# Performance work log

Measured on AMD Instinct MI355X. Metric: run time of the kernel, lower is better.

The kernel has to match this reference:

```python
import jax, jax.numpy as jnp
import numpy as np

B, F, T, H, K = 512, 64, 64, 512, 4  # batch, in_feat, timesteps, hidden, num cells (air0,bed0,air1,bed1)


def setup_inputs() -> dict:
    key = jax.random.key(0)
    ks = jax.random.split(key, 10)
    s = 1.0 / np.sqrt(H)
    u = lambda k, shape: jax.random.uniform(k, shape, jnp.float32, -s, s)
    return {
        "data": jax.random.normal(ks[0], (B, F, T), jnp.float32),
        "init": jax.random.normal(ks[1], (B, H), jnp.float32),
        # stacked params for the 4 branches in order [air0, bed0, air1, bed1]
        "fc_in_W": u(ks[2], (K, H, F)),
        "fc_in_b": u(ks[3], (K, H)),
        "Wih": u(ks[4], (K, 3 * H, H)),   # torch GRUCell weight_ih, gate order r,z,n
        "Whh": u(ks[5], (K, 3 * H, H)),
        "bih": u(ks[6], (K, 3 * H)),
        "bhh": u(ks[7], (K, 3 * H)),
        "fc_out_W": u(ks[8], (2, H)),     # [air, bed] output heads (Linear(512,1))
        "fc_out_b": u(ks[9], (2,)),
    }


def reference(data, init, fc_in_W, fc_in_b, Wih, Whh, bih, bhh, fc_out_W, fc_out_b):
    # Input projections (Linear + ReLU; Dropout is identity in eval): [T, K, B, H]
    proj = jax.nn.relu(jnp.einsum('bft,kof->tkbo', data, fc_in_W) + fc_in_b[None, :, None, :])
    # branches 2,3 (air1, bed1) consume the sequence reversed (data[:, :, 63-i])
    x_seq = jnp.concatenate([proj[:, :2], proj[::-1, 2:]], axis=1)  # [T, K, B, H]

    h0 = jnp.broadcast_to(init[None], (K,) + init.shape)  # all 4 cells start from init

    def step(h, x):  # h, x: [K, B, H]
        gi = jnp.einsum('kbi,koi->kbo', x, Wih) + bih[:, None, :]
        gh = jnp.einsum('kbi,koi->kbo', h, Whh) + bhh[:, None, :]
        ir, iz, inn = jnp.split(gi, 3, axis=-1)
        hr, hz, hn = jnp.split(gh, 3, axis=-1)
        r = jax.nn.sigmoid(ir + hr)
        z = jax.nn.sigmoid(iz + hz)
        n = jnp.tanh(inn + r * hn)
        h_new = (1.0 - z) * n + z * h
        return h_new, h_new

    _, hs = jax.lax.scan(step, h0, x_seq)  # [T, K, B, H]

    # output i (1..64) combines fwd hidden[i] with bwd hidden[65-i] -> reverse bwd stack
    air = hs[:, 0] + hs[::-1, 2]  # [T, B, H]
    bed = hs[:, 1] + hs[::-1, 3]
    air_out = (jnp.einsum('tbh,h->tb', air, fc_out_W[0]) + fc_out_b[0]).T  # [B, T]
    bed_out = (jnp.einsum('tbh,h->tb', bed, fc_out_W[1]) + fc_out_b[1]).T
    return air_out, bed_out
```

## Files before the change

### kernel.cpp

```cpp
#include <hip/hip_runtime.h>
#include <hip/hip_bf16.h>

typedef __hip_bfloat16 bf16;
typedef __attribute__((ext_vector_type(8))) short short8;
typedef __attribute__((ext_vector_type(4))) float f32x4;

#define Hdim 512
#define Bdim 512
#define Tdim 64
#define Fdim 64
#define NC   4

__device__ __forceinline__ float sigmoidf_(float x){ return 1.f/(1.f + __expf(-x)); }
__device__ __forceinline__ float tanhf_(float x){
  float t = __expf(-2.f*fabsf(x));
  float r = (1.f - t)/(1.f + t);
  return copysignf(r, x);
}
__device__ __forceinline__ float bf2f_(short u){
  return __uint_as_float(((unsigned)(unsigned short)u) << 16);
}
__device__ __forceinline__ short f2bf_(float f){
  bf16 b = (bf16)f;
  return *(short*)&b;
}

__global__ __launch_bounds__(256) void pack_kernel(const float* __restrict__ src,
                                                   bf16* __restrict__ dst, int n){
  int idx = (blockIdx.x*256 + threadIdx.x)*4;
  if (idx < n){
    float4 v = *(const float4*)(src + idx);
    dst[idx+0] = (bf16)v.x;
    dst[idx+1] = (bf16)v.y;
    dst[idx+2] = (bf16)v.z;
    dst[idx+3] = (bf16)v.w;
  }
}

__global__ __launch_bounds__(256) void transpose_kernel(const float* __restrict__ data,
                                                        bf16* __restrict__ dataT){
  __shared__ bf16 tile[64*65];
  int b = blockIdx.x;
  int tid = threadIdx.x;
  for (int i = 0; i < 16; ++i){
    int idx = tid + i*256;
    int f = idx >> 6, t = idx & 63;
    tile[f*65 + t] = (bf16)data[(b*64 + f)*64 + t];
  }
  __syncthreads();
  for (int i = 0; i < 16; ++i){
    int idx = tid + i*256;
    int t = idx >> 6, f = idx & 63;
    dataT[(t*Bdim + b)*64 + f] = tile[f*65 + t];
  }
}

__global__ __launch_bounds__(256) void init_kernel(const float* __restrict__ init_h,
                            bf16* __restrict__ h_b1, unsigned* __restrict__ flags){
  int idx = blockIdx.x*256 + threadIdx.x;
  int k = idx >> 18;
  int rem = idx & 262143;
  int bg = rem >> 9;
  int o  = rem & 511;
  int dst = ((k*2 + (bg >> 8))*16 + (o >> 5))*8192 + (bg & 255)*32 + (o & 31);
  h_b1[dst] = (bf16)init_h[rem];
  if (idx < 512) flags[idx] = 0u;
}

__global__ __launch_bounds__(256) void proj_kernel(const bf16* __restrict__ dataT,
    const bf16* __restrict__ fc_in_W, const float* __restrict__ fc_in_b,
    bf16* __restrict__ x_seq){
  __shared__ short ldsA[64*72];
  __shared__ short ldsW[128*72];
  int blk = blockIdx.x;
  int s  = blk >> 7;
  int k  = (blk >> 5) & 3;
  int bt = (blk >> 2) & 7;
  int on = blk & 3;
  int tid = threadIdx.x;
  int lane = tid & 63, wid = tid >> 6;
  int quad = lane >> 4, l16 = lane & 15;
  int src_t = (k < 2) ? s : (Tdim - 1 - s);

  const short* Ag = (const short*)(dataT + (src_t*Bdim + bt*64)*Fdim);
  #pragma unroll
  for (int i = 0; i < 2; ++i){
    int c = tid + i*256; int r = c >> 3, off = c & 7;
    *(int4*)(&ldsA[r*72 + off*8]) = *(const int4*)(&Ag[r*64 + off*8]);
  }
  const short* Wg = (const short*)(fc_in_W + (k*Hdim + on*128)*Fdim);
  #pragma unroll
  for (int i = 0; i < 4; ++i){
    int c = tid + i*256; int r = c >> 3, off = c & 7;
    *(int4*)(&ldsW[r*72 + off*8]) = *(const int4*)(&Wg[r*64 + off*8]);
  }
  __syncthreads();

  f32x4 acc[2][4];
  #pragma unroll
  for (int nt=0; nt<2; ++nt)
    #pragma unroll
    for (int rb=0; rb<4; ++rb) acc[nt][rb] = (f32x4){0.f,0.f,0.f,0.f};

  #pragma unroll
  for (int kk = 0; kk < 2; ++kk){
    int io = kk*32 + quad*8;
    short8 a[4];
    #pragma unroll
    for (int rb=0; rb<4; ++rb) a[rb] = *(const short8*)(&ldsA[(rb*16+l16)*72 + io]);
    #pragma unroll
    for (int nt=0; nt<2; ++nt){
      short8 bw = *(const short8*)(&ldsW[(wid*32 + nt*16 + l16)*72 + io]);
      #pragma unroll
      for (int rb=0; rb<4; ++rb)
        acc[nt][rb] = __builtin_amdgcn_mfma_f32_16x16x32_bf16(a[rb], bw, acc[nt][rb], 0,0,0);
    }
  }

  #pragma unroll
  for (int nt=0; nt<2; ++nt){
    int o = on*128 + wid*32 + nt*16 + l16;
    float bias = fc_in_b[k*Hdim + o];
    #pragma unroll
    for (int rb=0; rb<4; ++rb){
      #pragma unroll
      for (int reg=0; reg<4; ++reg){
        int b = bt*64 + rb*16 + quad*4 + reg;
        float v = acc[nt][rb][reg] + bias;
        v = v > 0.f ? v : 0.f;
        x_seq[((size_t)(s*NC + k)*Bdim + b)*Hdim + o] = (bf16)v;
      }
    }
  }
}

__global__ __launch_bounds__(512) void rnn_kernel(
    const bf16* __restrict__ x_seq, const float* __restrict__ init_h,
    bf16* __restrict__ h_b0, bf16* __restrict__ h_b1,
    const float* __restrict__ Wih, const float* __restrict__ Whh,
    const float* __restrict__ bih, const float* __restrict__ bhh,
    const float* __restrict__ fc_out_W,
    bf16* __restrict__ gi, float* __restrict__ part,
    unsigned* __restrict__ flags, unsigned* __restrict__ xslot)
{
  __shared__ short wlds[3*2*16*512];
  __shared__ int sslot;

  int tid = threadIdx.x;
  int lane = tid & 63, wid = tid >> 6;
  int quad = lane >> 4, l16 = lane & 15;

  unsigned xcc;
  asm volatile("s_getreg_b32 %0, hwreg(HW_REG_XCC_ID)" : "=s"(xcc));
  xcc &= 7u;
  if (tid == 0)
    sslot = (int)__hip_atomic_fetch_add(&xslot[xcc*32], 1u,
                __ATOMIC_RELAXED, __HIP_MEMORY_SCOPE_WORKGROUP);
  __syncthreads();
  int grp = (int)xcc;
  int k   = grp >> 1;
  int bt  = grp & 1;
  int slot = sslot & 31;
  int producer = (slot < 16);
  int j    = slot & 15;
  int obase = j*32;
  int rot  = j;
  unsigned* gflags = flags + grp*32;

  const float* Wsrc = producer ? Wih : Whh;
  for (int i = tid; i < 3*2*16*64; i += 512){
    int plane = i >> 11;
    int rem   = i & 2047;
    int nt    = rem >> 10;
    int rem2  = rem & 1023;
    int kc    = rem2 >> 6;
    int ln    = rem2 & 63;
    int ll16  = ln & 15, lq = ln >> 4;
    const float* srcp = Wsrc +
        ((size_t)(k*3 + plane)*Hdim + obase + nt*16 + ll16)*Hdim + kc*32 + lq*8;
    float4 f0 = *(const float4*)srcp;
    float4 f1 = *(const float4*)(srcp + 4);
    short8 pk;
    pk[0]=f2bf_(f0.x); pk[1]=f2bf_(f0.y); pk[2]=f2bf_(f0.z); pk[3]=f2bf_(f0.w);
    pk[4]=f2bf_(f1.x); pk[5]=f2bf_(f1.y); pk[6]=f2bf_(f1.z); pk[7]=f2bf_(f1.w);
    *(int4*)(&wlds[i*8]) = *(int4*)&pk;
  }

  #define GEMM32X(ABASE) do {                                                   \
    const short* ap0_ = (ABASE) + (wid*32 + l16)*Hdim + quad*8;                 \
    const short* ap1_ = ap0_ + 16*Hdim;                                         \
    short8 ab_[4][2];                                                           \
    _Pragma("unroll")                                                           \
    for (int d=0; d<4; ++d){                                                    \
      int c_ = (d + rot) & 15;                                                  \
      ab_[d][0] = *(const short8*)(ap0_ + c_*32);                               \
      ab_[d][1] = *(const short8*)(ap1_ + c_*32);                               \
    }                                                                           \
    short8 bb_[2][6];                                                           \
    _Pragma("unroll")                                                           \
    for (int p=0; p<6; ++p)                                                     \
      bb_[0][p] = *(const short8*)(&wlds[((p*16 + rot)<<9) + (lane<<3)]);       \
    _Pragma("unroll")                                                           \
    for (int kc=0; kc<16; ++kc){                                                \
      short8 a0_ = ab_[kc&3][0], a1_ = ab_[kc&3][1];                            \
      if (kc < 12){                                                             \
        int c_ = (kc + 4 + rot) & 15;                                           \
        ab_[kc&3][0] = *(const short8*)(ap0_ + c_*32);                          \
        ab_[kc&3][1] = *(const short8*)(ap1_ + c_*32);                          \
      }                                                                         \
      if (kc < 15){                                                             \
        int c_ = (kc + 1 + rot) & 15;                                           \
        _Pragma("unroll")                                                       \
        for (int p=0; p<6; ++p)                                                 \
          bb_[(kc+1)&1][p] = *(const short8*)(&wlds[((p*16 + c_)<<9) + (lane<<3)]); \
      }                                                                         \
      _Pragma("unroll")                                                         \
      for (int g=0; g<3; ++g){                                                  \
        _Pragma("unroll")                                                       \
        for (int nt=0; nt<2; ++nt){                                             \
          short8 bw_ = bb_[kc&1][g*2+nt];                                       \
          acc[g][nt][0] = __builtin_amdgcn_mfma_f32_16x16x32_bf16(a0_, bw_, acc[g][nt][0], 0,0,0); \
          acc[g][nt][1] = __builtin_amdgcn_mfma_f32_16x16x32_bf16(a1_, bw_, acc[g][nt][1], 0,0,0); \
        }                                                                       \
      }                                                                         \
    }                                                                           \
  } while(0)

  #define GEMM32H(HCB) do {                                                     \
    const short* hp0_ = (HCB) + (wid*32 + l16)*32 + quad*8;                     \
    const short* hp1_ = hp0_ + 16*32;                                           \
    short8 ab_[4][2];                                                           \
    _Pragma("unroll")                                                           \
    for (int d=0; d<4; ++d){                                                    \
      int c_ = (d + rot) & 15;                                                  \
      ab_[d][0] = *(const short8*)(hp0_ + c_*8192);                             \
      ab_[d][1] = *(const short8*)(hp1_ + c_*8192);                             \
    }                                                                           \
    short8 bb_[2][6];                                                           \
    _Pragma("unroll")                                                           \
    for (int p=0; p<6; ++p)                                                     \
      bb_[0][p] = *(const short8*)(&wlds[((p*16 + rot)<<9) + (lane<<3)]);       \
    _Pragma("unroll")                                                           \
    for (int kc=0; kc<16; ++kc){                                                \
      short8 a0_ = ab_[kc&3][0], a1_ = ab_[kc&3][1];                            \
      if (kc < 12){                                                             \
        int c_ = (kc + 4 + rot) & 15;                                           \
        ab_[kc&3][0] = *(const short8*)(hp0_ + c_*8192);                        \
        ab_[kc&3][1] = *(const short8*)(hp1_ + c_*8192);                        \
      }                                                                         \
      if (kc < 15){                                                             \
        int c_ = (kc + 1 + rot) & 15;                                           \
        _Pragma("unroll")                                                       \
        for (int p=0; p<6; ++p)                                                 \
          bb_[(kc+1)&1][p] = *(const short8*)(&wlds[((p*16 + c_)<<9) + (lane<<3)]); \
      }                                                                         \
      _Pragma("unroll")                                                         \
      for (int g=0; g<3; ++g){                                                  \
        _Pragma("unroll")                                                       \
        for (int nt=0; nt<2; ++nt){                                             \
          short8 bw_ = bb_[kc&1][g*2+nt];                                       \
          acc[g][nt][0] = __builtin_amdgcn_mfma_f32_16x16x32_bf16(a0_, bw_, acc[g][nt][0], 0,0,0); \
          acc[g][nt][1] = __builtin_amdgcn_mfma_f32_16x16x32_bf16(a1_, bw_, acc[g][nt][1], 0,0,0); \
        }                                                                       \
      }                                                                         \
    }                                                                           \
  } while(0)

  if (producer){
    __syncthreads();
    for (int s = 0; s < 64; ++s){
      f32x4 acc[3][2][2];
      #pragma unroll
      for (int g=0; g<3; ++g)
        #pragma unroll
        for (int nt=0; nt<2; ++nt){
          acc[g][nt][0] = (f32x4){0.f,0.f,0.f,0.f};
          acc[g][nt][1] = (f32x4){0.f,0.f,0.f,0.f};
        }
      if (s >= 3){
        if (wid == 0){
          int g_ = 0;
          while (__hip_atomic_load(&gflags[16 + j], __ATOMIC_RELAXED,
                                   __HIP_MEMORY_SCOPE_AGENT) < (unsigned)(s - 2)){
            __builtin_amdgcn_s_sleep(1);
            if (++g_ > 4000000) break;
          }
        }
        __syncthreads();
      }
      const short* x_base = (const short*)(x_seq + ((size_t)(s*NC + k)*Bdim + bt*256)*Hdim);
      GEMM32X(x_base);
      bf16* gb = gi + ((size_t)(((s % 3)*8 + grp)*16 + j))*24576;
      #pragma unroll
      for (int g=0; g<3; ++g){
        #pragma unroll
        for (int nt=0; nt<2; ++nt){
          short8 pk;
          #pragma unroll
          for (int rb=0; rb<2; ++rb)
            #pragma unroll
            for (int reg=0; reg<4; ++reg)
              pk[rb*4+reg] = f2bf_(acc[g][nt][rb][reg]);
          *(int4*)(gb + ((g*2+nt)*512 + wid*64 + lane)*8) = *(int4*)&pk;
        }
      }
      __syncthreads();
      if (tid == 0)
        __hip_atomic_fetch_add(&gflags[j], 1u,
                               __ATOMIC_RELAXED, __HIP_MEMORY_SCOPE_AGENT);
    }
  } else {
    int o0 = obase + l16, o1 = o0 + 16;
    float br0  = bih[k*3*Hdim + o0] + bhh[k*3*Hdim + o0];
    float br1  = bih[k*3*Hdim + o1] + bhh[k*3*Hdim + o1];
    float bz0  = bih[k*3*Hdim + Hdim + o0] + bhh[k*3*Hdim + Hdim + o0];
    float bz1  = bih[k*3*Hdim + Hdim + o1] + bhh[k*3*Hdim + Hdim + o1];
    float bnx0 = bih[k*3*Hdim + 2*Hdim + o0];
    float bnx1 = bih[k*3*Hdim + 2*Hdim + o1];
    float bnh0 = bhh[k*3*Hdim + 2*Hdim + o0];
    float bnh1 = bhh[k*3*Hdim + 2*Hdim + o1];
    float wout0 = fc_out_W[(k & 1)*Hdim + o0];
    float wout1 = fc_out_W[(k & 1)*Hdim + o1];

    float hk[2][2][4];
    #pragma unroll
    for (int nt=0; nt<2; ++nt)
      #pragma unroll
      for (int rb=0; rb<2; ++rb)
        #pragma unroll
        for (int reg=0; reg<4; ++reg)
          hk[nt][rb][reg] =
            init_h[(bt*256 + wid*32 + rb*16 + quad*4 + reg)*Hdim + obase + nt*16 + l16];

    __syncthreads();

    const int hgrp = (k*2 + bt)*16;

    for (int s = 0; s < 64; ++s){
      const bf16* h_in  = (s & 1) ? h_b0 : h_b1;
      bf16*       h_out = (s & 1) ? h_b1 : h_b0;

      f32x4 acc[3][2][2];
      #pragma unroll
      for (int g=0; g<3; ++g)
        #pragma unroll
        for (int nt=0; nt<2; ++nt){
          acc[g][nt][0] = (f32x4){0.f,0.f,0.f,0.f};
          acc[g][nt][1] = (f32x4){0.f,0.f,0.f,0.f};
        }

      {
        if (wid == 0){
          int g_ = 0;
          for (;;){
            unsigned v_ = 0xFFFFFFFFu, thr_ = 0u;
            if (lane < 16){
              v_ = __hip_atomic_load(&gflags[16 + lane], __ATOMIC_RELAXED,
                                     __HIP_MEMORY_SCOPE_AGENT);
              thr_ = (unsigned)s;
            } else if (lane == 16){
              v_ = __hip_atomic_load(&gflags[j], __ATOMIC_RELAXED,
                                     __HIP_MEMORY_SCOPE_AGENT);
              thr_ = (unsigned)(s + 1);
            }
            if (__ballot(v_ >= thr_) == ~0ull) break;
            __builtin_amdgcn_s_sleep(1);
            if (++g_ > 4000000) break;
          }
        }
        __syncthreads();
      }

      const bf16* gb = gi + ((size_t)(((s % 3)*8 + grp)*16 + j))*24576;
      short8 gv[6];
      #pragma unroll
      for (int p=0; p<6; ++p){
        int4 t = *(const int4*)(gb + (p*512 + wid*64 + lane)*8);
        gv[p] = *(short8*)&t;
      }

      const short* h_cb = (const short*)h_in + (size_t)hgrp*8192;
      GEMM32H(h_cb);

      float hnv[2][2][4];
      bf16* hob = h_out + (size_t)(hgrp + j)*8192;
      #pragma unroll
      for (int rb = 0; rb < 2; ++rb){
        #pragma unroll
        for (int reg = 0; reg < 4; ++reg){
          int bl = wid*32 + rb*16 + quad*4 + reg;
          #pragma unroll
          for (int nt = 0; nt < 2; ++nt){
            float gir = bf2f_(gv[0*2+nt][rb*4+reg]);
            float giz = bf2f_(gv[1*2+nt][rb*4+reg]);
            float gin = bf2f_(gv[2*2+nt][rb*4+reg]);
            float br  = nt ? br1 : br0,  bz = nt ? bz1 : bz0;
            float bnx = nt ? bnx1 : bnx0, bnh = nt ? bnh1 : bnh0;
            float r = sigmoidf_(gir + acc[0][nt][rb][reg] + br);
            float z = sigmoidf_(giz + acc[1][nt][rb][reg] + bz);
            float n = tanhf_(gin + bnx + r*(acc[2][nt][rb][reg] + bnh));
            float hn = (1.f - z)*n + z*hk[nt][rb][reg];
            hk[nt][rb][reg] = hn;
            hnv[nt][rb][reg] = hn;
            hob[bl*32 + nt*16 + l16] = (bf16)hn;
          }
        }
      }

      __syncthreads();
      if (tid == 0)
        __hip_atomic_fetch_add(&gflags[16 + j], 1u,
                               __ATOMIC_RELAXED, __HIP_MEMORY_SCOPE_AGENT);

      int tmap = (k < 2) ? s : (Tdim - 1 - s);
      #pragma unroll
      for (int rb = 0; rb < 2; ++rb){
        #pragma unroll
        for (int reg = 0; reg < 4; ++reg){
          int bl = wid*32 + rb*16 + quad*4 + reg;
          float v = hnv[0][rb][reg]*wout0 + hnv[1][rb][reg]*wout1;
          v += __shfl_xor(v, 1, 64);
          v += __shfl_xor(v, 2, 64);
          v += __shfl_xor(v, 4, 64);
          v += __shfl_xor(v, 8, 64);
          if (l16 == 0)
            __builtin_nontemporal_store(v,
              &part[((size_t)(k*Tdim + tmap)*16 + j)*Bdim + bt*256 + bl]);
        }
      }
    }
  }
  #undef GEMM32X
  #undef GEMM32H
}

__global__ __launch_bounds__(256) void finalize_kernel(const float* __restrict__ part,
                                const float* __restrict__ fc_out_b, float* __restrict__ out){
  int idx = blockIdx.x*256 + threadIdx.x;
  int head = idx >> 15;
  int b = (idx >> 6) & 511;
  int t = idx & 63;
  float v = fc_out_b[head];
  #pragma unroll
  for (int kk = 0; kk < 2; ++kk){
    const float* p = part + (size_t)((head + kk*2)*Tdim + t)*16*Bdim + b;
    #pragma unroll
    for (int jj = 0; jj < 16; ++jj)
      v += p[jj*Bdim];
  }
  out[idx] = v;
}

extern "C" void kernel_launch(void* const* d_in, const int* in_sizes, int n_in,
                              void* d_out, int out_size, void* d_ws, size_t ws_size,
                              hipStream_t stream){
  (void)in_sizes; (void)n_in; (void)out_size; (void)ws_size;
  const float* data     = (const float*)d_in[0];
  const float* init_h   = (const float*)d_in[1];
  const float* fc_in_W  = (const float*)d_in[2];
  const float* fc_in_b  = (const float*)d_in[3];
  const float* Wih      = (const float*)d_in[4];
  const float* Whh      = (const float*)d_in[5];
  const float* bih      = (const float*)d_in[6];
  const float* bhh      = (const float*)d_in[7];
  const float* fc_out_W = (const float*)d_in[8];
  const float* fc_out_b = (const float*)d_in[9];
  float* out = (float*)d_out;

  char* ws = (char*)d_ws;
  bf16*  x_seq   = (bf16*)ws;
  bf16*  h_b0    = (bf16*)(ws + 134217728);
  bf16*  h_b1    = (bf16*)(ws + 136314880);
  bf16*  gi      = (bf16*)(ws + 138412032);
  bf16*  dataT   = (bf16*)(ws + 138412032);
  float* part    = (float*)(ws + 157286400);
  bf16*  fcW_bf  = (bf16*)(ws + 165675008);
  unsigned* flags= (unsigned*)(ws + 165937152);
  unsigned* xslot= (unsigned*)(ws + 165938176);

  const int nFW = NC*Hdim*Fdim;
  hipLaunchKernelGGL(pack_kernel, dim3(nFW/1024), dim3(256), 0, stream, fc_in_W, fcW_bf, nFW);
  hipLaunchKernelGGL(init_kernel, dim3(4096), dim3(256), 0, stream, init_h, h_b1, flags);
  hipLaunchKernelGGL(transpose_kernel, dim3(512), dim3(256), 0, stream, data, dataT);
  hipLaunchKernelGGL(proj_kernel, dim3(8192), dim3(256), 0, stream, dataT, fcW_bf, fc_in_b, x_seq);
  hipLaunchKernelGGL(rnn_kernel, dim3(256), dim3(512), 0, stream,
      x_seq, init_h, h_b0, h_b1, Wih, Whh, bih, bhh, fc_out_W, gi, part, flags, xslot);
  hipLaunchKernelGGL(finalize_kernel, dim3(256), dim3(256), 0, stream, part, fc_out_b, out);
}
```

Before: 743.4 us.

## Retile GRU GEMM warps to 64 rows by 16 cols, shrink gi ring

Each warp now computes a 64-row by 16-column tile instead of 32 by 32. That makes each warp load 3 LDS weight fragments per k-chunk instead of 6, while the A-side register loads double. The gi buffer ring drops from three slots to two, which tightens the producer/consumer flag thresholds. The consumer now waits for its own gi slot before the hidden-state barrier and prefetches gi during that wait. The partial-output layout doubles to 32 slices, so the finalize reduction and the workspace offsets change to match.

```diff
diff --git a/kernel.cpp b/kernel.cpp
--- a/kernel.cpp
+++ b/kernel.cpp
@@ -3,6 +3,7 @@
 
 typedef __hip_bfloat16 bf16;
 typedef __attribute__((ext_vector_type(8))) short short8;
+typedef __attribute__((ext_vector_type(4))) short short4_t;
 typedef __attribute__((ext_vector_type(4))) float f32x4;
 
 #define Hdim 512
@@ -148,6 +149,8 @@
 
   int tid = threadIdx.x;
   int lane = tid & 63, wid = tid >> 6;
+  int wgrp = wid >> 2;
+  int wsub = wid & 3;
   int quad = lane >> 4, l16 = lane & 15;
 
   unsigned xcc;
@@ -186,102 +189,64 @@
     *(int4*)(&wlds[i*8]) = *(int4*)&pk;
   }
 
-  #define GEMM32X(ABASE) do {                                                   \
-    const short* ap0_ = (ABASE) + (wid*32 + l16)*Hdim + quad*8;                 \
-    const short* ap1_ = ap0_ + 16*Hdim;                                         \
-    short8 ab_[4][2];                                                           \
+  #define GEMMNT(APFX, ROWSTRIDE, CSTRIDE) do {                                 \
+    const short* ap_[4];                                                        \
+    _Pragma("unroll")                                                           \
+    for (int rb=0; rb<4; ++rb)                                                  \
+      ap_[rb] = (APFX) + (wsub*64 + rb*16 + l16)*(ROWSTRIDE) + quad*8;          \
+    short8 ab_[4][4];                                                           \
     _Pragma("unroll")                                                           \
     for (int d=0; d<4; ++d){                                                    \
       int c_ = (d + rot) & 15;                                                  \
-      ab_[d][0] = *(const short8*)(ap0_ + c_*32);                               \
-      ab_[d][1] = *(const short8*)(ap1_ + c_*32);                               \
+      _Pragma("unroll")                                                         \
+      for (int rb=0; rb<4; ++rb)                                                \
+        ab_[d][rb] = *(const short8*)(ap_[rb] + (size_t)c_*(CSTRIDE));          \
     }                                                                           \
-    short8 bb_[2][6];                                                           \
+    short8 bb_[2][3];                                                           \
     _Pragma("unroll")                                                           \
-    for (int p=0; p<6; ++p)                                                     \
-      bb_[0][p] = *(const short8*)(&wlds[((p*16 + rot)<<9) + (lane<<3)]);       \
+    for (int g=0; g<3; ++g)                                                     \
+      bb_[0][g] = *(const short8*)(&wlds[((((g*2+wgrp)*16) + rot)<<9) + (lane<<3)]); \
     _Pragma("unroll")                                                           \
     for (int kc=0; kc<16; ++kc){                                                \
-      short8 a0_ = ab_[kc&3][0], a1_ = ab_[kc&3][1];                            \
+      short8 a_[4];                                                             \
+      _Pragma("unroll")                                                         \
+      for (int rb=0; rb<4; ++rb) a_[rb] = ab_[kc&3][rb];                        \
       if (kc < 12){                                                             \
         int c_ = (kc + 4 + rot) & 15;                                           \
-        ab_[kc&3][0] = *(const short8*)(ap0_ + c_*32);                          \
-        ab_[kc&3][1] = *(const short8*)(ap1_ + c_*32);                          \
+        _Pragma("unroll")                                                       \
+        for (int rb=0; rb<4; ++rb)                                              \
+          ab_[kc&3][rb] = *(const short8*)(ap_[rb] + (size_t)c_*(CSTRIDE));     \
       }                                                                         \
       if (kc < 15){                                                             \
         int c_ = (kc + 1 + rot) & 15;                                           \
         _Pragma("unroll")                                                       \
-        for (int p=0; p<6; ++p)                                                 \
-          bb_[(kc+1)&1][p] = *(const short8*)(&wlds[((p*16 + c_)<<9) + (lane<<3)]); \
+        for (int g=0; g<3; ++g)                                                 \
+          bb_[(kc+1)&1][g] =                                                    \
+            *(const short8*)(&wlds[((((g*2+wgrp)*16) + c_)<<9) + (lane<<3)]);   \
       }                                                                         \
       _Pragma("unroll")                                                         \
       for (int g=0; g<3; ++g){                                                  \
+        short8 bw_ = bb_[kc&1][g];                                              \
         _Pragma("unroll")                                                       \
-        for (int nt=0; nt<2; ++nt){                                             \
-          short8 bw_ = bb_[kc&1][g*2+nt];                                       \
-          acc[g][nt][0] = __builtin_amdgcn_mfma_f32_16x16x32_bf16(a0_, bw_, acc[g][nt][0], 0,0,0); \
-          acc[g][nt][1] = __builtin_amdgcn_mfma_f32_16x16x32_bf16(a1_, bw_, acc[g][nt][1], 0,0,0); \
-        }                                                                       \
+        for (int rb=0; rb<4; ++rb)                                              \
+          acc[g][rb] = __builtin_amdgcn_mfma_f32_16x16x32_bf16(a_[rb], bw_, acc[g][rb], 0,0,0); \
       }                                                                         \
     }                                                                           \
   } while(0)
 
-  #define GEMM32H(HCB) do {                                                     \
-    const short* hp0_ = (HCB) + (wid*32 + l16)*32 + quad*8;                     \
-    const short* hp1_ = hp0_ + 16*32;                                           \
-    short8 ab_[4][2];                                                           \
-    _Pragma("unroll")                                                           \
-    for (int d=0; d<4; ++d){                                                    \
-      int c_ = (d + rot) & 15;                                                  \
-      ab_[d][0] = *(const short8*)(hp0_ + c_*8192);                             \
-      ab_[d][1] = *(const short8*)(hp1_ + c_*8192);                             \
-    }                                                                           \
-    short8 bb_[2][6];                                                           \
-    _Pragma("unroll")                                                           \
-    for (int p=0; p<6; ++p)                                                     \
-      bb_[0][p] = *(const short8*)(&wlds[((p*16 + rot)<<9) + (lane<<3)]);       \
-    _Pragma("unroll")                                                           \
-    for (int kc=0; kc<16; ++kc){                                                \
-      short8 a0_ = ab_[kc&3][0], a1_ = ab_[kc&3][1];                            \
-      if (kc < 12){                                                             \
-        int c_ = (kc + 4 + rot) & 15;                                           \
-        ab_[kc&3][0] = *(const short8*)(hp0_ + c_*8192);                        \
-        ab_[kc&3][1] = *(const short8*)(hp1_ + c_*8192);                        \
-      }                                                                         \
-      if (kc < 15){                                                             \
-        int c_ = (kc + 1 + rot) & 15;                                           \
-        _Pragma("unroll")                                                       \
-        for (int p=0; p<6; ++p)                                                 \
-          bb_[(kc+1)&1][p] = *(const short8*)(&wlds[((p*16 + c_)<<9) + (lane<<3)]); \
-      }                                                                         \
-      _Pragma("unroll")                                                         \
-      for (int g=0; g<3; ++g){                                                  \
-        _Pragma("unroll")                                                       \
-        for (int nt=0; nt<2; ++nt){                                             \
-          short8 bw_ = bb_[kc&1][g*2+nt];                                       \
-          acc[g][nt][0] = __builtin_amdgcn_mfma_f32_16x16x32_bf16(a0_, bw_, acc[g][nt][0], 0,0,0); \
-          acc[g][nt][1] = __builtin_amdgcn_mfma_f32_16x16x32_bf16(a1_, bw_, acc[g][nt][1], 0,0,0); \
-        }                                                                       \
-      }                                                                         \
-    }                                                                           \
-  } while(0)
-
   if (producer){
     __syncthreads();
     for (int s = 0; s < 64; ++s){
-      f32x4 acc[3][2][2];
+      f32x4 acc[3][4];
       #pragma unroll
       for (int g=0; g<3; ++g)
         #pragma unroll
-        for (int nt=0; nt<2; ++nt){
-          acc[g][nt][0] = (f32x4){0.f,0.f,0.f,0.f};
-          acc[g][nt][1] = (f32x4){0.f,0.f,0.f,0.f};
-        }
-      if (s >= 3){
+        for (int rb=0; rb<4; ++rb) acc[g][rb] = (f32x4){0.f,0.f,0.f,0.f};
+      if (s >= 2){
         if (wid == 0){
           int g_ = 0;
           while (__hip_atomic_load(&gflags[16 + j], __ATOMIC_RELAXED,
-                                   __HIP_MEMORY_SCOPE_AGENT) < (unsigned)(s - 2)){
+                                   __HIP_MEMORY_SCOPE_AGENT) < (unsigned)(s - 1)){
             __builtin_amdgcn_s_sleep(1);
             if (++g_ > 4000000) break;
           }
@@ -289,19 +254,16 @@
         __syncthreads();
       }
       const short* x_base = (const short*)(x_seq + ((size_t)(s*NC + k)*Bdim + bt*256)*Hdim);
-      GEMM32X(x_base);
-      bf16* gb = gi + ((size_t)(((s % 3)*8 + grp)*16 + j))*24576;
+      GEMMNT(x_base, Hdim, 32);
+      bf16* gb = gi + ((size_t)(((s & 1)*8 + grp)*16 + j))*24576;
       #pragma unroll
       for (int g=0; g<3; ++g){
         #pragma unroll
-        for (int nt=0; nt<2; ++nt){
-          short8 pk;
+        for (int rb=0; rb<4; ++rb){
+          short4_t pk;
           #pragma unroll
-          for (int rb=0; rb<2; ++rb)
-            #pragma unroll
-            for (int reg=0; reg<4; ++reg)
-              pk[rb*4+reg] = f2bf_(acc[g][nt][rb][reg]);
-          *(int4*)(gb + ((g*2+nt)*512 + wid*64 + lane)*8) = *(int4*)&pk;
+          for (int reg=0; reg<4; ++reg) pk[reg] = f2bf_(acc[g][rb][reg]);
+          *(int2*)(gb + ((((g*2+wgrp)*16) + wsub*4 + rb)*64 + lane)*4) = *(int2*)&pk;
         }
       }
       __syncthreads();
@@ -310,27 +272,19 @@
                                __ATOMIC_RELAXED, __HIP_MEMORY_SCOPE_AGENT);
     }
   } else {
-    int o0 = obase + l16, o1 = o0 + 16;
-    float br0  = bih[k*3*Hdim + o0] + bhh[k*3*Hdim + o0];
-    float br1  = bih[k*3*Hdim + o1] + bhh[k*3*Hdim + o1];
-    float bz0  = bih[k*3*Hdim + Hdim + o0] + bhh[k*3*Hdim + Hdim + o0];
-    float bz1  = bih[k*3*Hdim + Hdim + o1] + bhh[k*3*Hdim + Hdim + o1];
-    float bnx0 = bih[k*3*Hdim + 2*Hdim + o0];
-    float bnx1 = bih[k*3*Hdim + 2*Hdim + o1];
-    float bnh0 = bhh[k*3*Hdim + 2*Hdim + o0];
-    float bnh1 = bhh[k*3*Hdim + 2*Hdim + o1];
-    float wout0 = fc_out_W[(k & 1)*Hdim + o0];
-    float wout1 = fc_out_W[(k & 1)*Hdim + o1];
-
-    float hk[2][2][4];
-    #pragma unroll
-    for (int nt=0; nt<2; ++nt)
-      #pragma unroll
-      for (int rb=0; rb<2; ++rb)
-        #pragma unroll
-        for (int reg=0; reg<4; ++reg)
-          hk[nt][rb][reg] =
-            init_h[(bt*256 + wid*32 + rb*16 + quad*4 + reg)*Hdim + obase + nt*16 + l16];
+    int o = obase + wgrp*16 + l16;
+    float br  = bih[k*3*Hdim + o] + bhh[k*3*Hdim + o];
+    float bz  = bih[k*3*Hdim + Hdim + o] + bhh[k*3*Hdim + Hdim + o];
+    float bnx = bih[k*3*Hdim + 2*Hdim + o];
+    float bnh = bhh[k*3*Hdim + 2*Hdim + o];
+    float wout = fc_out_W[(k & 1)*Hdim + o];
+
+    float hk[4][4];
+    #pragma unroll
+    for (int rb=0; rb<4; ++rb)
+      #pragma unroll
+      for (int reg=0; reg<4; ++reg)
+        hk[rb][reg] = init_h[(bt*256 + wsub*64 + rb*16 + quad*4 + reg)*Hdim + o];
 
     __syncthreads();
 
@@ -340,30 +294,40 @@
       const bf16* h_in  = (s & 1) ? h_b0 : h_b1;
       bf16*       h_out = (s & 1) ? h_b1 : h_b0;
 
-      f32x4 acc[3][2][2];
+      f32x4 acc[3][4];
       #pragma unroll
       for (int g=0; g<3; ++g)
         #pragma unroll
-        for (int nt=0; nt<2; ++nt){
-          acc[g][nt][0] = (f32x4){0.f,0.f,0.f,0.f};
-          acc[g][nt][1] = (f32x4){0.f,0.f,0.f,0.f};
-        }
-
-      {
+        for (int rb=0; rb<4; ++rb) acc[g][rb] = (f32x4){0.f,0.f,0.f,0.f};
+
+      if (wid == 0){
+        int g_ = 0;
+        while (__hip_atomic_load(&gflags[j], __ATOMIC_RELAXED,
+                                 __HIP_MEMORY_SCOPE_AGENT) < (unsigned)(s + 1)){
+          __builtin_amdgcn_s_sleep(1);
+          if (++g_ > 4000000) break;
+        }
+      }
+      __syncthreads();
+      const bf16* gb = gi + ((size_t)(((s & 1)*8 + grp)*16 + j))*24576;
+      short4_t gv[3][4];
+      #pragma unroll
+      for (int g=0; g<3; ++g)
+        #pragma unroll
+        for (int rb=0; rb<4; ++rb){
+          int2 t = *(const int2*)(gb + ((((g*2+wgrp)*16) + wsub*4 + rb)*64 + lane)*4);
+          gv[g][rb] = *(short4_t*)&t;
+        }
+
+      if (s){
         if (wid == 0){
           int g_ = 0;
           for (;;){
-            unsigned v_ = 0xFFFFFFFFu, thr_ = 0u;
-            if (lane < 16){
+            unsigned v_ = 0xFFFFFFFFu;
+            if (lane < 16)
               v_ = __hip_atomic_load(&gflags[16 + lane], __ATOMIC_RELAXED,
                                      __HIP_MEMORY_SCOPE_AGENT);
-              thr_ = (unsigned)s;
-            } else if (lane == 16){
-              v_ = __hip_atomic_load(&gflags[j], __ATOMIC_RELAXED,
-                                     __HIP_MEMORY_SCOPE_AGENT);
-              thr_ = (unsigned)(s + 1);
-            }
-            if (__ballot(v_ >= thr_) == ~0ull) break;
+            if (__ballot(v_ >= (unsigned)s) == ~0ull) break;
             __builtin_amdgcn_s_sleep(1);
             if (++g_ > 4000000) break;
           }
@@ -371,39 +335,23 @@
         __syncthreads();
       }
 
-      const bf16* gb = gi + ((size_t)(((s % 3)*8 + grp)*16 + j))*24576;
-      short8 gv[6];
-      #pragma unroll
-      for (int p=0; p<6; ++p){
-        int4 t = *(const int4*)(gb + (p*512 + wid*64 + lane)*8);
-        gv[p] = *(short8*)&t;
-      }
-
       const short* h_cb = (const short*)h_in + (size_t)hgrp*8192;
-      GEMM32H(h_cb);
-
-      float hnv[2][2][4];
+      GEMMNT(h_cb, 32, 8192);
+
+      float hnv[4][4];
       bf16* hob = h_out + (size_t)(hgrp + j)*8192;
       #pragma unroll
-      for (int rb = 0; rb < 2; ++rb){
+      for (int rb = 0; rb < 4; ++rb){
         #pragma unroll
         for (int reg = 0; reg < 4; ++reg){
-          int bl = wid*32 + rb*16 + quad*4 + reg;
-          #pragma unroll
-          for (int nt = 0; nt < 2; ++nt){
-            float gir = bf2f_(gv[0*2+nt][rb*4+reg]);
-            float giz = bf2f_(gv[1*2+nt][rb*4+reg]);
-            float gin = bf2f_(gv[2*2+nt][rb*4+reg]);
-            float br  = nt ? br1 : br0,  bz = nt ? bz1 : bz0;
-            float bnx = nt ? bnx1 : bnx0, bnh = nt ? bnh1 : bnh0;
-            float r = sigmoidf_(gir + acc[0][nt][rb][reg] + br);
-            float z = sigmoidf_(giz + acc[1][nt][rb][reg] + bz);
-            float n = tanhf_(gin + bnx + r*(acc[2][nt][rb][reg] + bnh));
-            float hn = (1.f - z)*n + z*hk[nt][rb][reg];
-            hk[nt][rb][reg] = hn;
-            hnv[nt][rb][reg] = hn;
-            hob[bl*32 + nt*16 + l16] = (bf16)hn;
-          }
+          int bl = wsub*64 + rb*16 + quad*4 + reg;
+          float r = sigmoidf_(bf2f_(gv[0][rb][reg]) + acc[0][rb][reg] + br);
+          float z = sigmoidf_(bf2f_(gv[1][rb][reg]) + acc[1][rb][reg] + bz);
+          float n = tanhf_(bf2f_(gv[2][rb][reg]) + bnx + r*(acc[2][rb][reg] + bnh));
+          float hn = (1.f - z)*n + z*hk[rb][reg];
+          hk[rb][reg] = hn;
+          hnv[rb][reg] = hn;
+          hob[bl*32 + wgrp*16 + l16] = (bf16)hn;
         }
       }
 
@@ -414,24 +362,23 @@
 
       int tmap = (k < 2) ? s : (Tdim - 1 - s);
       #pragma unroll
-      for (int rb = 0; rb < 2; ++rb){
+      for (int rb = 0; rb < 4; ++rb){
         #pragma unroll
         for (int reg = 0; reg < 4; ++reg){
-          int bl = wid*32 + rb*16 + quad*4 + reg;
-          float v = hnv[0][rb][reg]*wout0 + hnv[1][rb][reg]*wout1;
+          int bl = wsub*64 + rb*16 + quad*4 + reg;
+          float v = hnv[rb][reg] * wout;
           v += __shfl_xor(v, 1, 64);
           v += __shfl_xor(v, 2, 64);
           v += __shfl_xor(v, 4, 64);
           v += __shfl_xor(v, 8, 64);
           if (l16 == 0)
             __builtin_nontemporal_store(v,
-              &part[((size_t)(k*Tdim + tmap)*16 + j)*Bdim + bt*256 + bl]);
+              &part[((size_t)(k*Tdim + tmap)*32 + j*2 + wgrp)*Bdim + bt*256 + bl]);
         }
       }
     }
   }
-  #undef GEMM32X
-  #undef GEMM32H
+  #undef GEMMNT
 }
 
 __global__ __launch_bounds__(256) void finalize_kernel(const float* __restrict__ part,
@@ -443,9 +390,9 @@
   float v = fc_out_b[head];
   #pragma unroll
   for (int kk = 0; kk < 2; ++kk){
-    const float* p = part + (size_t)((head + kk*2)*Tdim + t)*16*Bdim + b;
-    #pragma unroll
-    for (int jj = 0; jj < 16; ++jj)
+    const float* p = part + (size_t)((head + kk*2)*Tdim + t)*32*Bdim + b;
+    #pragma unroll
+    for (int jj = 0; jj < 32; ++jj)
       v += p[jj*Bdim];
   }
   out[idx] = v;
@@ -472,11 +419,11 @@
   bf16*  h_b0    = (bf16*)(ws + 134217728);
   bf16*  h_b1    = (bf16*)(ws + 136314880);
   bf16*  gi      = (bf16*)(ws + 138412032);
-  bf16*  dataT   = (bf16*)(ws + 138412032);
-  float* part    = (float*)(ws + 157286400);
-  bf16*  fcW_bf  = (bf16*)(ws + 165675008);
-  unsigned* flags= (unsigned*)(ws + 165937152);
-  unsigned* xslot= (unsigned*)(ws + 165938176);
+  float* part    = (float*)(ws + 150994944);
+  bf16*  dataT   = (bf16*)(ws + 150994944);
+  bf16*  fcW_bf  = (bf16*)(ws + 155189248);
+  unsigned* flags= (unsigned*)(ws + 167772160);
+  unsigned* xslot= (unsigned*)(ws + 167773184);
 
   const int nFW = NC*Hdim*Fdim;
   hipLaunchKernelGGL(pack_kernel, dim3(nFW/1024), dim3(256), 0, stream, fc_in_W, fcW_bf, nFW);
```

Result: slower. 1.210 ms (+62.8%).

## Replace block-wide barriers with per-wavefront flag synchronization in persistent GRU kernel

Applied to the files above, without the earlier changes.

The persistent RNN kernel now signals and waits on per-wave progress flags instead of doing __syncthreads plus a single-thread atomic per block, so each wavefront proceeds as soon as the specific data it needs is ready. The flag array is enlarged and relocated to hold per-wave counters, and init clears the larger range. Producer-side A-operand prefetch depth in the input GEMM grows from 4 to 6 stages. Relying on s_waitcnt vmcnt before relaxed atomics for ordering risks visibility problems, and the deeper prefetch uses more registers.

```diff
diff --git a/kernel.cpp b/kernel.cpp
--- a/kernel.cpp
+++ b/kernel.cpp
@@ -10,6 +10,8 @@
 #define Tdim 64
 #define Fdim 64
 #define NC   4
+
+#define WAITCNT_VM0 0x0F70
 
 __device__ __forceinline__ float sigmoidf_(float x){ return 1.f/(1.f + __expf(-x)); }
 __device__ __forceinline__ float tanhf_(float x){
@@ -64,7 +66,7 @@
   int o  = rem & 511;
   int dst = ((k*2 + (bg >> 8))*16 + (o >> 5))*8192 + (bg & 255)*32 + (o & 31);
   h_b1[dst] = (bf16)init_h[rem];
-  if (idx < 512) flags[idx] = 0u;
+  if (idx < 4352) flags[idx] = 0u;
 }
 
 __global__ __launch_bounds__(256) void proj_kernel(const bf16* __restrict__ dataT,
@@ -165,7 +167,7 @@
   int j    = slot & 15;
   int obase = j*32;
   int rot  = j;
-  unsigned* gflags = flags + grp*32;
+  unsigned* gflags = flags + grp*512;
 
   const float* Wsrc = producer ? Wih : Whh;
   for (int i = tid; i < 3*2*16*64; i += 512){
@@ -185,13 +187,14 @@
     pk[4]=f2bf_(f1.x); pk[5]=f2bf_(f1.y); pk[6]=f2bf_(f1.z); pk[7]=f2bf_(f1.w);
     *(int4*)(&wlds[i*8]) = *(int4*)&pk;
   }
+  __syncthreads();
 
   #define GEMM32X(ABASE) do {                                                   \
     const short* ap0_ = (ABASE) + (wid*32 + l16)*Hdim + quad*8;                 \
     const short* ap1_ = ap0_ + 16*Hdim;                                         \
-    short8 ab_[4][2];                                                           \
-    _Pragma("unroll")                                                           \
-    for (int d=0; d<4; ++d){                                                    \
+    short8 ab_[6][2];                                                           \
+    _Pragma("unroll")                                                           \
+    for (int d=0; d<6; ++d){                                                    \
       int c_ = (d + rot) & 15;                                                  \
       ab_[d][0] = *(const short8*)(ap0_ + c_*32);                               \
       ab_[d][1] = *(const short8*)(ap1_ + c_*32);                               \
@@ -202,11 +205,11 @@
       bb_[0][p] = *(const short8*)(&wlds[((p*16 + rot)<<9) + (lane<<3)]);       \
     _Pragma("unroll")                                                           \
     for (int kc=0; kc<16; ++kc){                                                \
-      short8 a0_ = ab_[kc&3][0], a1_ = ab_[kc&3][1];                            \
-      if (kc < 12){                                                             \
-        int c_ = (kc + 4 + rot) & 15;                                           \
-        ab_[kc&3][0] = *(const short8*)(ap0_ + c_*32);                          \
-        ab_[kc&3][1] = *(const short8*)(ap1_ + c_*32);                          \
+      short8 a0_ = ab_[kc%6][0], a1_ = ab_[kc%6][1];                            \
+      if (kc < 10){                                                             \
+        int c_ = (kc + 6 + rot) & 15;                                           \
+        ab_[kc%6][0] = *(const short8*)(ap0_ + c_*32);                          \
+        ab_[kc%6][1] = *(const short8*)(ap1_ + c_*32);                          \
       }                                                                         \
       if (kc < 15){                                                             \
         int c_ = (kc + 1 + rot) & 15;                                           \
@@ -233,8 +236,8 @@
     _Pragma("unroll")                                                           \
     for (int d=0; d<4; ++d){                                                    \
       int c_ = (d + rot) & 15;                                                  \
-      ab_[d][0] = *(const short8*)(hp0_ + c_*8192);                             \
-      ab_[d][1] = *(const short8*)(hp1_ + c_*8192);                             \
+      ab_[d][0] = *(const short8*)(hp0_ + (size_t)c_*8192);                     \
+      ab_[d][1] = *(const short8*)(hp1_ + (size_t)c_*8192);                     \
     }                                                                           \
     short8 bb_[2][6];                                                           \
     _Pragma("unroll")                                                           \
@@ -245,8 +248,8 @@
       short8 a0_ = ab_[kc&3][0], a1_ = ab_[kc&3][1];                            \
       if (kc < 12){                                                             \
         int c_ = (kc + 4 + rot) & 15;                                           \
-        ab_[kc&3][0] = *(const short8*)(hp0_ + c_*8192);                        \
-        ab_[kc&3][1] = *(const short8*)(hp1_ + c_*8192);                        \
+        ab_[kc&3][0] = *(const short8*)(hp0_ + (size_t)c_*8192);                \
+        ab_[kc&3][1] = *(const short8*)(hp1_ + (size_t)c_*8192);                \
       }                                                                         \
       if (kc < 15){                                                             \
         int c_ = (kc + 1 + rot) & 15;                                           \
@@ -266,8 +269,17 @@
     }                                                                           \
   } while(0)
 
+  #define WAITF(fidx, thr) do {                                                 \
+    int g_ = 0;                                                                 \
+    while (__hip_atomic_load(&gflags[fidx], __ATOMIC_RELAXED,                   \
+                             __HIP_MEMORY_SCOPE_AGENT) < (unsigned)(thr)){      \
+      __builtin_amdgcn_s_sleep(1);                                              \
+      if (++g_ > 4000000) break;                                                \
+    }                                                                           \
+    __asm__ __volatile__("" ::: "memory");                                      \
+  } while(0)
+
   if (producer){
-    __syncthreads();
     for (int s = 0; s < 64; ++s){
       f32x4 acc[3][2][2];
       #pragma unroll
@@ -277,17 +289,7 @@
           acc[g][nt][0] = (f32x4){0.f,0.f,0.f,0.f};
           acc[g][nt][1] = (f32x4){0.f,0.f,0.f,0.f};
         }
-      if (s >= 3){
-        if (wid == 0){
-          int g_ = 0;
-          while (__hip_atomic_load(&gflags[16 + j], __ATOMIC_RELAXED,
-                                   __HIP_MEMORY_SCOPE_AGENT) < (unsigned)(s - 2)){
-            __builtin_amdgcn_s_sleep(1);
-            if (++g_ > 4000000) break;
-          }
-        }
-        __syncthreads();
-      }
+      if (s >= 3) WAITF(256 + wid*16 + j, s - 2);
       const short* x_base = (const short*)(x_seq + ((size_t)(s*NC + k)*Bdim + bt*256)*Hdim);
       GEMM32X(x_base);
       bf16* gb = gi + ((size_t)(((s % 3)*8 + grp)*16 + j))*24576;
@@ -304,9 +306,9 @@
           *(int4*)(gb + ((g*2+nt)*512 + wid*64 + lane)*8) = *(int4*)&pk;
         }
       }
-      __syncthreads();
-      if (tid == 0)
-        __hip_atomic_fetch_add(&gflags[j], 1u,
+      __builtin_amdgcn_s_waitcnt(WAITCNT_VM0);
+      if (lane == 0)
+        __hip_atomic_fetch_add(&gflags[wid*16 + j], 1u,
                                __ATOMIC_RELAXED, __HIP_MEMORY_SCOPE_AGENT);
     }
   } else {
@@ -332,8 +334,6 @@
           hk[nt][rb][reg] =
             init_h[(bt*256 + wid*32 + rb*16 + quad*4 + reg)*Hdim + obase + nt*16 + l16];
 
-    __syncthreads();
-
     const int hgrp = (k*2 + bt)*16;
 
     for (int s = 0; s < 64; ++s){
@@ -349,27 +349,7 @@
           acc[g][nt][1] = (f32x4){0.f,0.f,0.f,0.f};
         }
 
-      {
-        if (wid == 0){
-          int g_ = 0;
-          for (;;){
-            unsigned v_ = 0xFFFFFFFFu, thr_ = 0u;
-            if (lane < 16){
-              v_ = __hip_atomic_load(&gflags[16 + lane], __ATOMIC_RELAXED,
-                                     __HIP_MEMORY_SCOPE_AGENT);
-              thr_ = (unsigned)s;
-            } else if (lane == 16){
-              v_ = __hip_atomic_load(&gflags[j], __ATOMIC_RELAXED,
-                                     __HIP_MEMORY_SCOPE_AGENT);
-              thr_ = (unsigned)(s + 1);
-            }
-            if (__ballot(v_ >= thr_) == ~0ull) break;
-            __builtin_amdgcn_s_sleep(1);
-            if (++g_ > 4000000) break;
-          }
-        }
-        __syncthreads();
-      }
+      WAITF(wid*16 + j, s + 1);
 
       const bf16* gb = gi + ((size_t)(((s % 3)*8 + grp)*16 + j))*24576;
       short8 gv[6];
@@ -377,6 +357,20 @@
       for (int p=0; p<6; ++p){
         int4 t = *(const int4*)(gb + (p*512 + wid*64 + lane)*8);
         gv[p] = *(short8*)&t;
+      }
+
+      if (s){
+        int g_ = 0;
+        for (;;){
+          unsigned v_ = 0xFFFFFFFFu;
+          if (lane < 16)
+            v_ = __hip_atomic_load(&gflags[256 + wid*16 + lane], __ATOMIC_RELAXED,
+                                   __HIP_MEMORY_SCOPE_AGENT);
+          if (__ballot(v_ >= (unsigned)s) == ~0ull) break;
+          __builtin_amdgcn_s_sleep(1);
+          if (++g_ > 4000000) break;
+        }
+        __asm__ __volatile__("" ::: "memory");
       }
 
       const short* h_cb = (const short*)h_in + (size_t)hgrp*8192;
@@ -407,9 +401,9 @@
         }
       }
 
-      __syncthreads();
-      if (tid == 0)
-        __hip_atomic_fetch_add(&gflags[16 + j], 1u,
+      __builtin_amdgcn_s_waitcnt(WAITCNT_VM0);
+      if (lane == 0)
+        __hip_atomic_fetch_add(&gflags[256 + wid*16 + j], 1u,
                                __ATOMIC_RELAXED, __HIP_MEMORY_SCOPE_AGENT);
 
       int tmap = (k < 2) ? s : (Tdim - 1 - s);
@@ -432,6 +426,7 @@
   }
   #undef GEMM32X
   #undef GEMM32H
+  #undef WAITF
 }
 
 __global__ __launch_bounds__(256) void finalize_kernel(const float* __restrict__ part,
@@ -476,7 +471,7 @@
   float* part    = (float*)(ws + 157286400);
   bf16*  fcW_bf  = (bf16*)(ws + 165675008);
   unsigned* flags= (unsigned*)(ws + 165937152);
-  unsigned* xslot= (unsigned*)(ws + 165938176);
+  unsigned* xslot= (unsigned*)(ws + 165953536);
 
   const int nFW = NC*Hdim*Fdim;
   hipLaunchKernelGGL(pack_kernel, dim3(nFW/1024), dim3(256), 0, stream, fc_in_W, fcW_bf, nFW);
```

Result: slower. 1.561 ms (+110.0%).
